# Optimization experiments

Hardware: AMD Instinct MI355X
Metric: run time of the kernel (lower is better)

The kernel has to match this reference:

```python
import jax, jax.numpy as jnp
import numpy as np

NUM_MIXTURES = 10
DIM_INPUT = 512
DIM_FEATURES = 512
SEQ_LEN = 512
BATCH = 16
NUM_CHAR = 1024
DIM_CONTEXT = 256


def setup_inputs() -> dict:
    key = jax.random.key(0)
    ks = jax.random.split(key, 6)
    inputs = jax.random.normal(ks[0], (SEQ_LEN, BATCH, DIM_INPUT), dtype=jnp.float32)
    context_vectors = jax.random.normal(ks[1], (NUM_CHAR, BATCH, DIM_CONTEXT), dtype=jnp.float32)
    init_means = jnp.zeros((BATCH, NUM_MIXTURES), dtype=jnp.float32)
    # StackedLinearLayers params: 2 layers, leaky_relu between, out dim = 3*K
    s1 = 1.0 / np.sqrt(DIM_INPUT)
    s2 = 1.0 / np.sqrt(DIM_FEATURES)
    W1 = jax.random.uniform(ks[2], (DIM_INPUT, DIM_FEATURES), jnp.float32, -s1, s1)
    b1 = jax.random.uniform(ks[3], (DIM_FEATURES,), jnp.float32, -s1, s1)
    W2 = jax.random.uniform(ks[4], (DIM_FEATURES, 3 * NUM_MIXTURES), jnp.float32, -s2, s2)
    b2 = jax.random.uniform(ks[5], (3 * NUM_MIXTURES,), jnp.float32, -s2, s2)
    return dict(inputs=inputs, context_vectors=context_vectors, init_means=init_means,
                W1=W1, b1=b1, W2=W2, b2=b2, extra_chars=0)


def reference(inputs, context_vectors, init_means, W1, b1, W2, b2, extra_chars):
    K = NUM_MIXTURES
    seq_len, batch, _ = inputs.shape
    num_char = context_vectors.shape[0]
    total_char = num_char + extra_chars

    # StackedLinearLayers: leaky_relu MLP, last layer linear -> (S, B, 3K)
    h = jax.nn.leaky_relu(inputs @ W1 + b1, negative_slope=0.01)
    outs = h @ W2 + b2
    outs = jax.nn.softplus(outs)  # pos_fun = softplus

    delta_means, vars_, weights = jnp.split(outs, 3, axis=2)  # each (S, B, K)
    delta_means = delta_means / 25.0
    vars_ = jnp.clip(vars_, 0.01, 100.0)
    means = jnp.cumsum(delta_means, axis=0) + init_means[None, :, :]  # (S, B, K)

    cidxs = jnp.arange(total_char, dtype=jnp.float32)  # (T,)
    # dists: (S, B, K, T)
    dists = -((means[..., None] - cidxs) ** 2) * vars_[..., None]
    # attn_weights = exp(logsumexp over mixtures)
    attn_weights = jnp.exp(
        jax.scipy.special.logsumexp(jnp.log(weights)[..., None] + dists, axis=2)
    )  # (S, B, T)

    # attended contexts: (S, B, D)
    attn_contexts = jnp.einsum('sbc,cbd->sbd', attn_weights[:, :, :num_char], context_vectors)
    return attn_contexts, attn_weights, means, vars_, weights
```

## Files before the change

### kernel.cpp

```cpp
#include <hip/hip_runtime.h>
#include <math.h>

#define S_LEN 512
#define BATCH 16
#define DIN   512
#define DF    512
#define NMIX  10
#define NCHAR 1024
#define DCTX  256
#define M_ROWS (S_LEN*BATCH)

#define OFF_CTXOUT 0
#define OFF_ATTN   (S_LEN*BATCH*DCTX)
#define OFF_MEANS  (OFF_ATTN + S_LEN*BATCH*NCHAR)
#define OFF_VARS   (OFF_MEANS + S_LEN*BATCH*NMIX)
#define OFF_WTS    (OFF_VARS  + S_LEN*BATCH*NMIX)

#define WS_XH    0
#define WS_W1T   (8u<<20)
#define WS_W2T   (9u<<20)
#define WS_HH    (10u<<20)
#define WS_DM    (26u<<20)

#define NX4     1048576
#define CVT_BLOCKS (NX4/256)
#define W1T_BLOCKS 64
#define W2T_BLOCKS 64

typedef float    f32x16 __attribute__((ext_vector_type(16)));
typedef float    f32x4v __attribute__((ext_vector_type(4)));
typedef _Float16 f16x8  __attribute__((ext_vector_type(8)));

__device__ __forceinline__ unsigned short f2h(float x) {
    union { _Float16 h; unsigned short u; } cv;
    cv.h = (_Float16)x;
    return cv.u;
}
__device__ __forceinline__ ushort4 cvt4(float4 v) {
    ushort4 o; o.x = f2h(v.x); o.y = f2h(v.y); o.z = f2h(v.z); o.w = f2h(v.w);
    return o;
}
__device__ __forceinline__ void nt_store4(float* p, float a, float b, float c, float d) {
    f32x4v v; v.x = a; v.y = b; v.z = c; v.w = d;
    __builtin_nontemporal_store(v, (f32x4v*)p);
}

__global__ __launch_bounds__(256) void convert_kernel(
    const float* __restrict__ X, const float* __restrict__ W1,
    const float* __restrict__ W2,
    unsigned short* __restrict__ Xh, unsigned short* __restrict__ W1T,
    float* __restrict__ W2T)
{
    const int bid = blockIdx.x;
    const int tid = threadIdx.x;
    if (bid < CVT_BLOCKS) {
        const int i4 = bid*256 + tid;
        ((ushort4*)Xh)[i4] = cvt4(((const float4*)X)[i4]);
    } else if (bid < CVT_BLOCKS + W1T_BLOCKS) {
        __shared__ unsigned short tile[64*68];
        const int b2 = bid - CVT_BLOCKS;
        const int k0 = (b2 >> 3) * 64, n0 = (b2 & 7) * 64;
        #pragma unroll
        for (int q = 0; q < 4; q++) {
            const int r = q*16 + (tid >> 4);
            const int c = (tid & 15) * 4;
            float4 v = *(const float4*)(W1 + (size_t)(k0+r)*DF + n0 + c);
            *(ushort4*)(tile + r*68 + c) = cvt4(v);
        }
        __syncthreads();
        #pragma unroll
        for (int q = 0; q < 4; q++) {
            const int n  = q*16 + (tid >> 4);
            const int kq = (tid & 15) * 4;
            ushort4 o;
            o.x = tile[(kq+0)*68 + n];
            o.y = tile[(kq+1)*68 + n];
            o.z = tile[(kq+2)*68 + n];
            o.w = tile[(kq+3)*68 + n];
            *(ushort4*)(W1T + (size_t)(n0+n)*DIN + k0 + kq) = o;
        }
    } else {
        const int idx = (bid - CVT_BLOCKS - W1T_BLOCKS)*256 + tid;
        if (idx < 512*32) {
            const int j = idx >> 9, k = idx & 511;
            W2T[idx] = (j < 30) ? W2[k*30 + j] : 0.f;
        }
    }
}

__global__ __launch_bounds__(256) void gemm1_kernel(
    const unsigned short* __restrict__ Xh, const unsigned short* __restrict__ W1T,
    const float* __restrict__ b1, unsigned short* __restrict__ Hh)
{
    __shared__ __align__(16) unsigned short As[64*72];
    __shared__ __align__(16) unsigned short Bs[64*72];
    const int row0 = (blockIdx.x >> 3) * 64;
    const int n0   = (blockIdx.x & 7)  * 64;
    const int tid  = threadIdx.x;
    const int lane = tid & 63, w = tid >> 6;
    const int wr = (w >> 1) * 32, wc = (w & 1) * 32;
    const int m  = lane & 31,  g  = lane >> 5;
    const int sa = tid >> 2,   ka = (tid & 3) * 16;

    f32x16 acc = {};
    const unsigned short* aptr = Xh  + (size_t)(row0+sa)*DIN + ka;
    const unsigned short* bptr = W1T + (size_t)(n0 +sa)*DIN + ka;

    for (int kt = 0; kt < DIN; kt += 64) {
        uint4 av0 = *(const uint4*)(aptr + kt);
        uint4 av1 = *(const uint4*)(aptr + kt + 8);
        uint4 bv0 = *(const uint4*)(bptr + kt);
        uint4 bv1 = *(const uint4*)(bptr + kt + 8);
        __syncthreads();
        *(uint4*)(As + sa*72 + ka)     = av0;
        *(uint4*)(As + sa*72 + ka + 8) = av1;
        *(uint4*)(Bs + sa*72 + ka)     = bv0;
        *(uint4*)(Bs + sa*72 + ka + 8) = bv1;
        __syncthreads();
        #pragma unroll
        for (int ks = 0; ks < 64; ks += 16) {
            f16x8 af = *(const f16x8*)(As + (wr+m)*72 + ks + g*8);
            f16x8 bf = *(const f16x8*)(Bs + (wc+m)*72 + ks + g*8);
            acc = __builtin_amdgcn_mfma_f32_32x32x16_f16(af, bf, acc, 0, 0, 0);
        }
    }
    const int ncol = n0 + wc + m;
    const float bb = b1[ncol];
    #pragma unroll
    for (int r = 0; r < 16; r++) {
        const int rowloc = (r & 3) + 8*(r >> 2) + 4*g;
        const int row = row0 + wr + rowloc;
        float v = acc[r] + bb;
        v = v > 0.f ? v : 0.01f * v;
        Hh[(size_t)row*DF + ncol] = f2h(v);
    }
}

__global__ __launch_bounds__(256) void gemm2_kernel(
    const unsigned short* __restrict__ Hh, const float* __restrict__ W2T,
    const float* __restrict__ b2,
    float* __restrict__ dm_ws, float* __restrict__ dvars, float* __restrict__ dwts)
{
    __shared__ __align__(16) unsigned short Hs[32*520];
    const int tid = threadIdx.x;
    const int r0  = blockIdx.x * 32;
    {
        const uint4* src = (const uint4*)(Hh + (size_t)r0*DF);
        #pragma unroll
        for (int i = 0; i < 8; i++) {
            int u   = tid + i*256;
            int row = u >> 6;
            int col = (u & 63) * 8;
            *(uint4*)(Hs + row*520 + col) = src[u];
        }
    }
    __syncthreads();

    const int r  = tid & 31;
    const int j0 = tid >> 5;
    const unsigned short* hrow = Hs + r*520;
    float acc[4] = {0.f, 0.f, 0.f, 0.f};

    for (int k0 = 0; k0 < DF; k0 += 8) {
        union { uint4 u; _Float16 h[8]; } hv;
        hv.u = *(const uint4*)(hrow + k0);
        float wv[4][8];
        #pragma unroll
        for (int q = 0; q < 4; q++) {
            *(float4*)(wv[q])     = *(const float4*)(W2T + (size_t)(j0 + q*8)*DF + k0);
            *(float4*)(wv[q] + 4) = *(const float4*)(W2T + (size_t)(j0 + q*8)*DF + k0 + 4);
        }
        #pragma unroll
        for (int i = 0; i < 8; i++) {
            float hf = (float)hv.h[i];
            acc[0] = fmaf(hf, wv[0][i], acc[0]);
            acc[1] = fmaf(hf, wv[1][i], acc[1]);
            acc[2] = fmaf(hf, wv[2][i], acc[2]);
            acc[3] = fmaf(hf, wv[3][i], acc[3]);
        }
    }
    const int row = r0 + r;
    #pragma unroll
    for (int q = 0; q < 4; q++) {
        const int j = j0 + q*8;
        if (j >= 30) continue;
        float dot = acc[q] + b2[j];
        float sp  = fmaxf(dot, 0.f) + log1pf(__expf(-fabsf(dot)));
        if (j < 10) {
            const int bb = row & (BATCH-1), s = row >> 4;
            dm_ws[((size_t)bb*NMIX + j)*S_LEN + s] = sp * (1.f/25.f);
        }
        else if (j < 20)  dvars[row*NMIX + (j-10)] = fminf(fmaxf(sp, 0.01f), 100.f);
        else              dwts [row*NMIX + (j-20)] = sp;
    }
}

__global__ __launch_bounds__(256) void fused_kernel(
    const float* __restrict__ dm_ws, const float* __restrict__ init_means,
    const float* __restrict__ vars_g, const float* __restrict__ wts_g,
    const float* __restrict__ ctx,
    float* __restrict__ means_out, float* __restrict__ attn_out,
    float* __restrict__ ctxout)
{
    __shared__ float mlds[320];
    __shared__ float vlds[320];
    __shared__ float wlds[320];
    __shared__ float redbuf[4];
    __shared__ __align__(16) unsigned short As[32*72];
    __shared__ __align__(16) unsigned short Bs[256*72];

    const int bid = blockIdx.x;
    const int b   = bid >> 4;
    const int s0  = (bid & 15) * 32;
    const int tid = threadIdx.x;
    const int lane = tid & 63, w = tid >> 6;
    const int m = lane & 31, g = lane >> 5;

    for (int k = w; k < NMIX; k += 4) {
        const float* chain = dm_ws + ((size_t)b*NMIX + k)*S_LEN;
        float part = 0.f;
        for (int s = lane; s < s0; s += 64) part += chain[s];
        #pragma unroll
        for (int d = 32; d >= 1; d >>= 1) part += __shfl_xor(part, d, 64);
        const float carry = init_means[b*NMIX + k] + part;
        float v = (lane < 32) ? chain[s0 + lane] : 0.f;
        #pragma unroll
        for (int d = 1; d < 32; d <<= 1) {
            float t = __shfl_up(v, d, 64);
            if (lane >= d) v += t;
        }
        if (lane < 32) mlds[lane*NMIX + k] = carry + v;
    }
    for (int idx = tid; idx < 320; idx += 256) {
        const int s = idx / NMIX, k = idx - s*NMIX;
        const int row = (s0 + s)*BATCH + b;
        vlds[idx] = vars_g[row*NMIX + k];
        wlds[idx] = wts_g [row*NMIX + k];
    }
    __syncthreads();

    float reach = 0.f;
    for (int idx = tid; idx < 320; idx += 256) {
        const int s = idx / NMIX, k = idx - s*NMIX;
        means_out[((s0 + s)*BATCH + b)*NMIX + k] = mlds[idx];
        reach = fmaxf(reach, mlds[idx] + 4.8f * rsqrtf(vlds[idx]));
    }
    #pragma unroll
    for (int d = 32; d >= 1; d >>= 1) reach = fmaxf(reach, __shfl_xor(reach, d, 64));
    if (lane == 0) redbuf[w] = reach;
    __syncthreads();
    const float rmax = fmaxf(fmaxf(redbuf[0], redbuf[1]),
                             fmaxf(redbuf[2], redbuf[3]));
    const int kmax = min(NCHAR, (((int)rmax) + 64) & ~63);

    const int r  = tid >> 3;
    const int c0 = (tid & 7) * 8;
    float mr[NMIX], vr[NMIX], wr_[NMIX];
    #pragma unroll
    for (int k = 0; k < NMIX; k++) {
        mr[k]  = mlds[r*NMIX + k];
        vr[k]  = vlds[r*NMIX + k];
        wr_[k] = wlds[r*NMIX + k];
    }
    const size_t arow = (size_t)((s0 + r)*BATCH + b) * NCHAR;

    const int tb = tid & 63, dseg = tid >> 6;
    const float* cbase = ctx + (size_t)b*DCTX + dseg*64;

    f32x16 acc0 = {}, acc1 = {};
    for (int kt = 0; kt < kmax; kt += 64) {
        float o[8];
        #pragma unroll
        for (int i = 0; i < 8; i++) {
            const float t = (float)(kt + c0 + i);
            float sum = 0.f;
            #pragma unroll
            for (int k = 0; k < NMIX; k++) {
                float d = t - mr[k];
                sum += wr_[k] * __expf(-d*d*vr[k]);
            }
            o[i] = sum;
        }
        __syncthreads();
        nt_store4(attn_out + arow + kt + c0,     o[0], o[1], o[2], o[3]);
        nt_store4(attn_out + arow + kt + c0 + 4, o[4], o[5], o[6], o[7]);
        {
            ushort4 h0, h1;
            h0.x = f2h(o[0]); h0.y = f2h(o[1]); h0.z = f2h(o[2]); h0.w = f2h(o[3]);
            h1.x = f2h(o[4]); h1.y = f2h(o[5]); h1.z = f2h(o[6]); h1.w = f2h(o[7]);
            *(ushort4*)(As + r*72 + c0)     = h0;
            *(ushort4*)(As + r*72 + c0 + 4) = h1;
        }
        {
            const float* p = cbase + (size_t)(kt + tb)*(BATCH*DCTX);
            #pragma unroll
            for (int e = 0; e < 4; e++) {
                float4 f0 = *(const float4*)(p + e*16);
                float4 f1 = *(const float4*)(p + e*16 + 4);
                float4 f2 = *(const float4*)(p + e*16 + 8);
                float4 f3 = *(const float4*)(p + e*16 + 12);
                ushort4 h0 = cvt4(f0), h1 = cvt4(f1), h2 = cvt4(f2), h3 = cvt4(f3);
                const int db = dseg*64 + e*16;
                Bs[(db + 0)*72 + tb] = h0.x;  Bs[(db + 1)*72 + tb] = h0.y;
                Bs[(db + 2)*72 + tb] = h0.z;  Bs[(db + 3)*72 + tb] = h0.w;
                Bs[(db + 4)*72 + tb] = h1.x;  Bs[(db + 5)*72 + tb] = h1.y;
                Bs[(db + 6)*72 + tb] = h1.z;  Bs[(db + 7)*72 + tb] = h1.w;
                Bs[(db + 8)*72 + tb] = h2.x;  Bs[(db + 9)*72 + tb] = h2.y;
                Bs[(db +10)*72 + tb] = h2.z;  Bs[(db +11)*72 + tb] = h2.w;
                Bs[(db +12)*72 + tb] = h3.x;  Bs[(db +13)*72 + tb] = h3.y;
                Bs[(db +14)*72 + tb] = h3.z;  Bs[(db +15)*72 + tb] = h3.w;
            }
        }
        __syncthreads();
        #pragma unroll
        for (int ks = 0; ks < 64; ks += 16) {
            f16x8 af  = *(const f16x8*)(As + m*72 + ks + g*8);
            f16x8 bf0 = *(const f16x8*)(Bs + (w*64 + m)*72      + ks + g*8);
            f16x8 bf1 = *(const f16x8*)(Bs + (w*64 + 32 + m)*72 + ks + g*8);
            acc0 = __builtin_amdgcn_mfma_f32_32x32x16_f16(af, bf0, acc0, 0, 0, 0);
            acc1 = __builtin_amdgcn_mfma_f32_32x32x16_f16(af, bf1, acc1, 0, 0, 0);
        }
    }
    for (int t = kmax + c0; t < NCHAR; t += 64) {
        nt_store4(attn_out + arow + t,     0.f, 0.f, 0.f, 0.f);
        nt_store4(attn_out + arow + t + 4, 0.f, 0.f, 0.f, 0.f);
    }

    #pragma unroll
    for (int rr = 0; rr < 16; rr++) {
        const int rowloc = (rr & 3) + 8*(rr >> 2) + 4*g;
        const int s = s0 + rowloc;
        float* op = ctxout + ((size_t)s*BATCH + b)*DCTX + w*64 + m;
        __builtin_nontemporal_store(acc0[rr], op);
        __builtin_nontemporal_store(acc1[rr], op + 32);
    }
}

extern "C" void kernel_launch(void* const* d_in, const int* in_sizes, int n_in,
                              void* d_out, int out_size, void* d_ws, size_t ws_size,
                              hipStream_t stream)
{
    const float* X     = (const float*)d_in[0];
    const float* ctx   = (const float*)d_in[1];
    const float* initm = (const float*)d_in[2];
    const float* W1    = (const float*)d_in[3];
    const float* b1    = (const float*)d_in[4];
    const float* W2    = (const float*)d_in[5];
    const float* b2    = (const float*)d_in[6];

    float* out      = (float*)d_out;
    float* out_ctx  = out + OFF_CTXOUT;
    float* out_attn = out + OFF_ATTN;
    float* out_mean = out + OFF_MEANS;
    float* out_var  = out + OFF_VARS;
    float* out_wts  = out + OFF_WTS;

    char* ws = (char*)d_ws;
    unsigned short* Xh   = (unsigned short*)(ws + WS_XH);
    unsigned short* W1T  = (unsigned short*)(ws + WS_W1T);
    float*          W2T  = (float*)         (ws + WS_W2T);
    unsigned short* Hh   = (unsigned short*)(ws + WS_HH);
    float*          dmws = (float*)         (ws + WS_DM);

    convert_kernel<<<CVT_BLOCKS + W1T_BLOCKS + W2T_BLOCKS, 256, 0, stream>>>(
        X, W1, W2, Xh, W1T, W2T);
    gemm1_kernel<<<(M_ROWS/64)*(DF/64), 256, 0, stream>>>(Xh, W1T, b1, Hh);
    gemm2_kernel<<<M_ROWS/32, 256, 0, stream>>>(Hh, W2T, b2, dmws, out_var, out_wts);
    fused_kernel<<<BATCH*16, 256, 0, stream>>>(dmws, initm, out_var, out_wts, ctx,
                                               out_mean, out_attn, out_ctx);
}
```

Measured before the change: 145.7 us.

## Enlarge gemm1 tiles to 128x128 with direct global-to-LDS loads and XOR swizzle

The first GEMM moves from 64x64 to 128x128 block tiles, with each wave computing a 64x64 sub-tile through four MFMA accumulators. Operands now go straight from global memory into LDS via global_load_lds instead of through registers, and an XOR swizzle replaces padding to avoid bank conflicts. The aim is more operand reuse per LDS load and less load/store instruction overhead. In exchange the grid shrinks to 256 blocks and each thread holds more accumulator registers.

```diff
diff --git a/kernel.cpp b/kernel.cpp
--- a/kernel.cpp
+++ b/kernel.cpp
@@ -43,6 +43,15 @@
 __device__ __forceinline__ void nt_store4(float* p, float a, float b, float c, float d) {
     f32x4v v; v.x = a; v.y = b; v.z = c; v.w = d;
     __builtin_nontemporal_store(v, (f32x4v*)p);
+}
+
+typedef __attribute__((address_space(1))) const unsigned int ga_u32;
+typedef __attribute__((address_space(3))) unsigned int ls_u32;
+__device__ __forceinline__ void gload_lds16(const unsigned short* g, unsigned short* l) {
+    __builtin_amdgcn_global_load_lds(
+        (ga_u32*)(unsigned long long)(const void*)g,
+        (ls_u32*)(unsigned int)(unsigned long long)(void*)l,
+        16, 0, 0);
 }
 
 __global__ __launch_bounds__(256) void convert_kernel(
@@ -92,47 +101,57 @@
     const unsigned short* __restrict__ Xh, const unsigned short* __restrict__ W1T,
     const float* __restrict__ b1, unsigned short* __restrict__ Hh)
 {
-    __shared__ __align__(16) unsigned short As[64*72];
-    __shared__ __align__(16) unsigned short Bs[64*72];
-    const int row0 = (blockIdx.x >> 3) * 64;
-    const int n0   = (blockIdx.x & 7)  * 64;
+    __shared__ __align__(16) unsigned short As[128*64];
+    __shared__ __align__(16) unsigned short Bs[128*64];
+    const int row0 = (blockIdx.x >> 2) * 128;
+    const int n0   = (blockIdx.x & 3)  * 128;
     const int tid  = threadIdx.x;
     const int lane = tid & 63, w = tid >> 6;
-    const int wr = (w >> 1) * 32, wc = (w & 1) * 32;
-    const int m  = lane & 31,  g  = lane >> 5;
-    const int sa = tid >> 2,   ka = (tid & 3) * 16;
-
-    f32x16 acc = {};
-    const unsigned short* aptr = Xh  + (size_t)(row0+sa)*DIN + ka;
-    const unsigned short* bptr = W1T + (size_t)(n0 +sa)*DIN + ka;
+    const int wr2 = (w >> 1) * 64, wc2 = (w & 1) * 64;
+    const int m  = lane & 31, g = lane >> 5;
+    const int szm = (m & 7) << 3;
+
+    const int lr = lane >> 3;
+    const int lc = ((lane & 7) ^ lr) * 8;
+    const unsigned short* aS = Xh  + (size_t)(row0 + w*32 + lr)*DIN + lc;
+    const unsigned short* bS = W1T + (size_t)(n0   + w*32 + lr)*DIN + lc;
+
+    f32x16 acc00 = {}, acc01 = {}, acc10 = {}, acc11 = {};
 
     for (int kt = 0; kt < DIN; kt += 64) {
-        uint4 av0 = *(const uint4*)(aptr + kt);
-        uint4 av1 = *(const uint4*)(aptr + kt + 8);
-        uint4 bv0 = *(const uint4*)(bptr + kt);
-        uint4 bv1 = *(const uint4*)(bptr + kt + 8);
-        __syncthreads();
-        *(uint4*)(As + sa*72 + ka)     = av0;
-        *(uint4*)(As + sa*72 + ka + 8) = av1;
-        *(uint4*)(Bs + sa*72 + ka)     = bv0;
-        *(uint4*)(Bs + sa*72 + ka + 8) = bv1;
+        #pragma unroll
+        for (int q = 0; q < 4; q++) {
+            gload_lds16(aS + (size_t)(q*8)*DIN + kt, As + (w*4 + q)*512);
+            gload_lds16(bS + (size_t)(q*8)*DIN + kt, Bs + (w*4 + q)*512);
+        }
         __syncthreads();
         #pragma unroll
         for (int ks = 0; ks < 64; ks += 16) {
-            f16x8 af = *(const f16x8*)(As + (wr+m)*72 + ks + g*8);
-            f16x8 bf = *(const f16x8*)(Bs + (wc+m)*72 + ks + g*8);
-            acc = __builtin_amdgcn_mfma_f32_32x32x16_f16(af, bf, acc, 0, 0, 0);
-        }
-    }
-    const int ncol = n0 + wc + m;
-    const float bb = b1[ncol];
+            const int ac = ks + g*8;
+            f16x8 a0 = *(const f16x8*)(As + (wr2      + m)*64 + (ac ^ szm));
+            f16x8 a1 = *(const f16x8*)(As + (wr2 + 32 + m)*64 + (ac ^ szm));
+            f16x8 b0 = *(const f16x8*)(Bs + (wc2      + m)*64 + (ac ^ szm));
+            f16x8 b1v= *(const f16x8*)(Bs + (wc2 + 32 + m)*64 + (ac ^ szm));
+            acc00 = __builtin_amdgcn_mfma_f32_32x32x16_f16(a0, b0,  acc00, 0, 0, 0);
+            acc01 = __builtin_amdgcn_mfma_f32_32x32x16_f16(a0, b1v, acc01, 0, 0, 0);
+            acc10 = __builtin_amdgcn_mfma_f32_32x32x16_f16(a1, b0,  acc10, 0, 0, 0);
+            acc11 = __builtin_amdgcn_mfma_f32_32x32x16_f16(a1, b1v, acc11, 0, 0, 0);
+        }
+        __syncthreads();
+    }
+
+    const int nc = n0 + wc2 + m;
+    const float bb0 = b1[nc], bb1 = b1[nc + 32];
     #pragma unroll
     for (int r = 0; r < 16; r++) {
         const int rowloc = (r & 3) + 8*(r >> 2) + 4*g;
-        const int row = row0 + wr + rowloc;
-        float v = acc[r] + bb;
-        v = v > 0.f ? v : 0.01f * v;
-        Hh[(size_t)row*DF + ncol] = f2h(v);
+        const int rA = row0 + wr2 + rowloc;
+        const int rB = rA + 32;
+        float v;
+        v = acc00[r] + bb0; v = v > 0.f ? v : 0.01f*v; Hh[(size_t)rA*DF + nc]      = f2h(v);
+        v = acc01[r] + bb1; v = v > 0.f ? v : 0.01f*v; Hh[(size_t)rA*DF + nc + 32] = f2h(v);
+        v = acc10[r] + bb0; v = v > 0.f ? v : 0.01f*v; Hh[(size_t)rB*DF + nc]      = f2h(v);
+        v = acc11[r] + bb1; v = v > 0.f ? v : 0.01f*v; Hh[(size_t)rB*DF + nc + 32] = f2h(v);
     }
 }
 
@@ -364,7 +383,7 @@
 
     convert_kernel<<<CVT_BLOCKS + W1T_BLOCKS + W2T_BLOCKS, 256, 0, stream>>>(
         X, W1, W2, Xh, W1T, W2T);
-    gemm1_kernel<<<(M_ROWS/64)*(DF/64), 256, 0, stream>>>(Xh, W1T, b1, Hh);
+    gemm1_kernel<<<(M_ROWS/128)*(DF/128), 256, 0, stream>>>(Xh, W1T, b1, Hh);
     gemm2_kernel<<<M_ROWS/32, 256, 0, stream>>>(Hh, W2T, b2, dmws, out_var, out_wts);
     fused_kernel<<<BATCH*16, 256, 0, stream>>>(dmws, initm, out_var, out_wts, ctx,
                                                out_mean, out_attn, out_ctx);
```

After: 144.5 us. Within noise of the previous version (-0.8%).
